# Kernel optimization log

Measured on AMD Instinct MI355X. Metric: run time of the kernel, lower is better.

Reference implementation:

```python
import jax, jax.numpy as jnp
import numpy as np

M, IN, OUT = 8192, 4096, 4096
BLOCK_N, BLOCK_K = 128, 128
NB = IN // BLOCK_K  # 32 in-blocks
INT8_MAX = 127.0
EPS = 1e-6


def setup_inputs() -> dict:
    key = jax.random.key(0)
    k1, k2, k3, k4 = jax.random.split(key, 4)
    x = jax.random.normal(k1, (M, IN), dtype=jnp.float32)
    # pre-quantized int8 weights, layout [output_size, input_size]
    weight_q = jax.random.randint(k2, (OUT, IN), -128, 128, dtype=jnp.int8)
    # block-wise scales, kernel-ready layout [in_blocks, 1, output_size]
    weight_scale = (jax.random.uniform(k3, (NB, 1, OUT), dtype=jnp.float32) + 0.5) * 0.01
    bias = jax.random.normal(k4, (OUT,), dtype=jnp.float32)
    return {"x": x, "weight_q": weight_q, "weight_scale": weight_scale, "bias": bias}


def _quantize_activation(x):
    # dynamic per-token symmetric int8 quantization
    amax = jnp.max(jnp.abs(x), axis=-1, keepdims=True)          # [M, 1]
    x_scale = jnp.maximum(amax, EPS) / INT8_MAX                  # [M, 1]
    x_q = jnp.clip(jnp.round(x / x_scale), -128.0, 127.0)        # [M, IN]
    return x_q, x_scale


def reference(x, weight_q, weight_scale, bias):
    # x: [M, IN]; weight_q: [OUT, IN] int8; weight_scale: [NB, 1, OUT]; bias: [OUT]
    x_q, x_scale = _quantize_activation(x)
    # Dequantize weights block-wise along K: scale for column k, row n is
    # weight_scale[k // BLOCK_K, 0, n].
    ws = weight_scale[:, 0, :].T                                 # [OUT, NB]
    w_deq = (weight_q.astype(jnp.float32).reshape(OUT, NB, BLOCK_K)
             * ws[:, :, None]).reshape(OUT, IN)                  # [OUT, IN] fp32
    # quantized matmul + dequant by activation scale
    out = jnp.einsum('mk,nk->mn', x_q, w_deq) * x_scale          # [M, OUT]
    out = out + bias
    return out
```

## Files before the change

### kernel.cpp

```cpp
#include <hip/hip_runtime.h>
#include <cstdint>

#define M_DIM 8192
#define K_DIM 4096
#define N_DIM 4096
#define NKT   32

typedef int   v4i  __attribute__((ext_vector_type(4)));
typedef int   v16i __attribute__((ext_vector_type(16)));
typedef float v4f  __attribute__((ext_vector_type(4)));

__device__ __forceinline__ void gload_lds16(const void* g, void* l) {
  __builtin_amdgcn_global_load_lds(
      (const __attribute__((address_space(1))) void*)g,
      (__attribute__((address_space(3))) void*)l, 16, 0, 0);
}

__global__ __launch_bounds__(256) void pack_w(
    const int* __restrict__ w32, int* __restrict__ w8) {
  const size_t i = (size_t)blockIdx.x * 256 + threadIdx.x;
  const int4 v = ((const int4*)w32)[i];
  w8[i] = (v.x & 255) | ((v.y & 255) << 8) | ((v.z & 255) << 16) | ((v.w & 255) << 24);
}

__global__ __launch_bounds__(256) void quant_rows(
    const float* __restrict__ x, int8_t* __restrict__ xq, float* __restrict__ xs) {
  const int row = blockIdx.x;
  const int tid = threadIdx.x;
  const float4* xr = (const float4*)(x + (size_t)row * K_DIM);

  float4 v[4];
  float amax = 0.f;
#pragma unroll
  for (int i = 0; i < 4; ++i) {
    v[i] = xr[i * 256 + tid];
    amax = fmaxf(amax, fmaxf(fmaxf(fabsf(v[i].x), fabsf(v[i].y)),
                             fmaxf(fabsf(v[i].z), fabsf(v[i].w))));
  }
#pragma unroll
  for (int off = 32; off > 0; off >>= 1)
    amax = fmaxf(amax, __shfl_xor(amax, off, 64));

  __shared__ float red[4];
  if ((tid & 63) == 0) red[tid >> 6] = amax;
  __syncthreads();
  amax = fmaxf(fmaxf(red[0], red[1]), fmaxf(red[2], red[3]));
  amax = fmaxf(amax, 1e-6f);
  const float s   = amax / 127.0f;
  const float inv = 127.0f / amax;
  if (tid == 0) xs[row] = s;

  int* xqo = (int*)(xq + (size_t)row * K_DIM);
#pragma unroll
  for (int i = 0; i < 4; ++i) {
    int q0 = (int)fminf(fmaxf(rintf(v[i].x * inv), -128.f), 127.f);
    int q1 = (int)fminf(fmaxf(rintf(v[i].y * inv), -128.f), 127.f);
    int q2 = (int)fminf(fmaxf(rintf(v[i].z * inv), -128.f), 127.f);
    int q3 = (int)fminf(fmaxf(rintf(v[i].w * inv), -128.f), 127.f);
    xqo[i * 256 + tid] =
        (q0 & 255) | ((q1 & 255) << 8) | ((q2 & 255) << 16) | ((q3 & 255) << 24);
  }
}

__global__ __launch_bounds__(512, 2) void gemm_q8(
    const int8_t* __restrict__ xq, const int8_t* __restrict__ wq,
    const float* __restrict__ wscale, const float* __restrict__ xs,
    const float* __restrict__ bias, float* __restrict__ out) {
  __shared__ int8_t lA[2][32768];
  __shared__ int8_t lB[2][32768];

  const int tid = threadIdx.x;
  const int m0 = blockIdx.x * 256;
  const int n0 = blockIdx.y * 256;

  const int srow   = tid >> 3;
  const int schunk = (tid & 7) ^ (srow & 7);
  const int8_t* ga = xq + (size_t)(m0 + srow) * K_DIM + schunk * 16;
  const int8_t* gb = wq + (size_t)(n0 + srow) * K_DIM + schunk * 16;

  const int lane = tid & 63;
  const int wv  = tid >> 6;
  const int wm  = (wv >> 2) << 7;
  const int wn  = (wv & 3) << 6;
  const int l31 = lane & 31;
  const int hi  = lane >> 5;

  int swz[4];
#pragma unroll
  for (int k = 0; k < 4; ++k) swz[k] = (((2 * k + hi) ^ (lane & 7)) << 4);
  const int aoff = (wm + l31) << 7;
  const int boff = (wn + l31) << 7;

  float facc[4][2][16];
#pragma unroll
  for (int i = 0; i < 4; ++i)
#pragma unroll
    for (int j = 0; j < 2; ++j)
#pragma unroll
      for (int r = 0; r < 16; ++r) facc[i][j][r] = 0.f;

  const float* wsp = wscale + n0 + wn + l31;

#pragma unroll
  for (int h = 0; h < 2; ++h)
#pragma unroll
    for (int p = 0; p < 2; ++p) {
      const size_t go = (size_t)(h * 128 + p * 64) * K_DIM;
      const int lo = h * 16384 + p * 8192 + tid * 16;
      gload_lds16(ga + go, &lA[0][lo]);
      gload_lds16(gb + go, &lB[0][lo]);
    }
  __syncthreads();

  for (int kt = 0; kt < NKT; ++kt) {
    const int d = kt & 1;
    const int kn = (kt + 1) & (NKT - 1);
    const int8_t* gan = ga + (size_t)kn * 128;
    const int8_t* gbn = gb + (size_t)kn * 128;
    int8_t* lan = &lA[d ^ 1][0];
    int8_t* lbn = &lB[d ^ 1][0];
    const int8_t* pa = &lA[d][0];
    const int8_t* pb = &lB[d][0];

    const float ws0 = wsp[(size_t)kt * N_DIM];
    const float ws1 = wsp[(size_t)kt * N_DIM + 32];

    v4i bfr[2][4];
#pragma unroll
    for (int j = 0; j < 2; ++j)
#pragma unroll
      for (int k = 0; k < 4; ++k)
        bfr[j][k] = *(const v4i*)(pb + boff + j * 4096 + swz[k]);

    v4i acur[4];
#pragma unroll
    for (int k = 0; k < 4; ++k)
      acur[k] = *(const v4i*)(pa + aoff + swz[k]);

#pragma unroll
    for (int h = 0; h < 2; ++h)
#pragma unroll
      for (int p = 0; p < 2; ++p) {
        const size_t go = (size_t)(h * 128 + p * 64) * K_DIM;
        const int lo = h * 16384 + p * 8192 + tid * 16;
        gload_lds16(gan + go, lan + lo);
        gload_lds16(gbn + go, lbn + lo);
      }

#pragma unroll
    for (int i = 0; i < 4; ++i) {
      v4i anxt[4];
      if (i < 3) {
#pragma unroll
        for (int k = 0; k < 4; ++k)
          anxt[k] = *(const v4i*)(pa + aoff + (i + 1) * 4096 + swz[k]);
      }

      v16i ic0 = {};
      v16i ic1 = {};
      __builtin_amdgcn_s_setprio(1);
#pragma unroll
      for (int k = 0; k < 4; ++k) {
        ic0 = __builtin_amdgcn_mfma_i32_32x32x32_i8(acur[k], bfr[0][k], ic0, 0, 0, 0);
        ic1 = __builtin_amdgcn_mfma_i32_32x32x32_i8(acur[k], bfr[1][k], ic1, 0, 0, 0);
      }
      __builtin_amdgcn_s_setprio(0);

#pragma unroll
      for (int r = 0; r < 16; ++r) facc[i][0][r] += ws0 * (float)ic0[r];
#pragma unroll
      for (int r = 0; r < 16; ++r) facc[i][1][r] += ws1 * (float)ic1[r];

      if (i < 3) {
#pragma unroll
        for (int k = 0; k < 4; ++k) acur[k] = anxt[k];
      }
    }

    __syncthreads();
  }

  const float bv0 = bias[n0 + wn + l31];
  const float bv1 = bias[n0 + wn + 32 + l31];
#pragma unroll
  for (int i = 0; i < 4; ++i) {
    const int rbase = m0 + wm + i * 32 + (hi << 2);
#pragma unroll
    for (int q = 0; q < 4; ++q) {
      const v4f xv = *(const v4f*)(xs + rbase + q * 8);
#pragma unroll
      for (int r4 = 0; r4 < 4; ++r4) {
        const int r = q * 4 + r4;
        float* op = out + (size_t)(rbase + q * 8 + r4) * N_DIM + n0 + wn + l31;
        op[0]  = facc[i][0][r] * xv[r4] + bv0;
        op[32] = facc[i][1][r] * xv[r4] + bv1;
      }
    }
  }
}

extern "C" void kernel_launch(void* const* d_in, const int* in_sizes, int n_in,
                              void* d_out, int out_size, void* d_ws, size_t ws_size,
                              hipStream_t stream) {
  const float* x      = (const float*)d_in[0];
  const int*   w32    = (const int*)d_in[1];
  const float* wscale = (const float*)d_in[2];
  const float* bias   = (const float*)d_in[3];
  float* out = (float*)d_out;

  int8_t* xq  = (int8_t*)d_ws;
  int8_t* wq8 = (int8_t*)d_ws + (size_t)M_DIM * K_DIM;
  float*  xs  = (float*)((char*)d_ws + (size_t)M_DIM * K_DIM + (size_t)N_DIM * K_DIM);

  pack_w<<<(N_DIM * (size_t)K_DIM / 4 + 255) / 256, 256, 0, stream>>>(w32, (int*)wq8);
  quant_rows<<<M_DIM, 256, 0, stream>>>(x, xq, xs);
  dim3 grid(M_DIM / 256, N_DIM / 256);
  gemm_q8<<<grid, 512, 0, stream>>>(xq, wq8, wscale, xs, bias, out);
}
```

Before: 440.0 us.

## Pre-swizzle operands into MFMA fragment layout and load B directly to registers

```diff
diff --git a/kernel.cpp b/kernel.cpp
--- a/kernel.cpp
+++ b/kernel.cpp
@@ -16,49 +16,65 @@
       (__attribute__((address_space(3))) void*)l, 16, 0, 0);
 }
 
-__global__ __launch_bounds__(256) void pack_w(
-    const int* __restrict__ w32, int* __restrict__ w8) {
-  const size_t i = (size_t)blockIdx.x * 256 + threadIdx.x;
-  const int4 v = ((const int4*)w32)[i];
-  w8[i] = (v.x & 255) | ((v.y & 255) << 8) | ((v.z & 255) << 16) | ((v.w & 255) << 24);
-}
-
-__global__ __launch_bounds__(256) void quant_rows(
-    const float* __restrict__ x, int8_t* __restrict__ xq, float* __restrict__ xs) {
-  const int row = blockIdx.x;
+
+__global__ __launch_bounds__(256) void prep(
+    const float* __restrict__ x, const int* __restrict__ w32,
+    int8_t* __restrict__ xq, float* __restrict__ xs, int8_t* __restrict__ wq) {
   const int tid = threadIdx.x;
-  const float4* xr = (const float4*)(x + (size_t)row * K_DIM);
-
-  float4 v[4];
-  float amax = 0.f;
-#pragma unroll
-  for (int i = 0; i < 4; ++i) {
-    v[i] = xr[i * 256 + tid];
-    amax = fmaxf(amax, fmaxf(fmaxf(fabsf(v[i].x), fabsf(v[i].y)),
-                             fmaxf(fabsf(v[i].z), fabsf(v[i].w))));
-  }
-#pragma unroll
-  for (int off = 32; off > 0; off >>= 1)
-    amax = fmaxf(amax, __shfl_xor(amax, off, 64));
-
-  __shared__ float red[4];
-  if ((tid & 63) == 0) red[tid >> 6] = amax;
-  __syncthreads();
-  amax = fmaxf(fmaxf(red[0], red[1]), fmaxf(red[2], red[3]));
-  amax = fmaxf(amax, 1e-6f);
-  const float s   = amax / 127.0f;
-  const float inv = 127.0f / amax;
-  if (tid == 0) xs[row] = s;
-
-  int* xqo = (int*)(xq + (size_t)row * K_DIM);
-#pragma unroll
-  for (int i = 0; i < 4; ++i) {
-    int q0 = (int)fminf(fmaxf(rintf(v[i].x * inv), -128.f), 127.f);
-    int q1 = (int)fminf(fmaxf(rintf(v[i].y * inv), -128.f), 127.f);
-    int q2 = (int)fminf(fmaxf(rintf(v[i].z * inv), -128.f), 127.f);
-    int q3 = (int)fminf(fmaxf(rintf(v[i].w * inv), -128.f), 127.f);
-    xqo[i * 256 + tid] =
-        (q0 & 255) | ((q1 & 255) << 8) | ((q2 & 255) << 16) | ((q3 & 255) << 24);
+  if (blockIdx.x < M_DIM) {
+    const int row = blockIdx.x;
+    const float4* xr = (const float4*)(x + (size_t)row * K_DIM);
+    float4 v[4];
+    float amax = 0.f;
+#pragma unroll
+    for (int i = 0; i < 4; ++i) {
+      v[i] = xr[tid * 4 + i];
+      amax = fmaxf(amax, fmaxf(fmaxf(fabsf(v[i].x), fabsf(v[i].y)),
+                               fmaxf(fabsf(v[i].z), fabsf(v[i].w))));
+    }
+#pragma unroll
+    for (int off = 32; off > 0; off >>= 1)
+      amax = fmaxf(amax, __shfl_xor(amax, off, 64));
+    __shared__ float red[4];
+    if ((tid & 63) == 0) red[tid >> 6] = amax;
+    __syncthreads();
+    amax = fmaxf(fmaxf(red[0], red[1]), fmaxf(red[2], red[3]));
+    amax = fmaxf(amax, 1e-6f);
+    const float s   = amax / 127.0f;
+    const float inv = 127.0f / amax;
+    if (tid == 0) xs[row] = s;
+
+    int w[4];
+#pragma unroll
+    for (int i = 0; i < 4; ++i) {
+      int q0 = (int)fminf(fmaxf(rintf(v[i].x * inv), -128.f), 127.f);
+      int q1 = (int)fminf(fmaxf(rintf(v[i].y * inv), -128.f), 127.f);
+      int q2 = (int)fminf(fmaxf(rintf(v[i].z * inv), -128.f), 127.f);
+      int q3 = (int)fminf(fmaxf(rintf(v[i].w * inv), -128.f), 127.f);
+      w[i] = (q0 & 255) | ((q1 & 255) << 8) | ((q2 & 255) << 16) | ((q3 & 255) << 24);
+    }
+    const int kt = tid >> 3, c = tid & 7;
+    const size_t doff =
+        ((((size_t)(row >> 5) * 32 + kt) * 4 + (c >> 1)) * 64 + (row & 31) + 32 * (c & 1)) * 16;
+    v4i ov = {w[0], w[1], w[2], w[3]};
+    *(v4i*)(xq + doff) = ov;
+  } else {
+    const size_t t = (size_t)(blockIdx.x - M_DIM) * 256 + tid;
+    const int l   = (int)(t & 63);
+    const int k   = (int)((t >> 6) & 3);
+    const int kt  = (int)((t >> 8) & 31);
+    const int n32 = (int)(t >> 13);
+    const int row = n32 * 32 + (l & 31);
+    const int col = kt * 128 + (2 * k + (l >> 5)) * 16;
+    const int4* src = (const int4*)(w32 + (size_t)row * K_DIM + col);
+    int o[4];
+#pragma unroll
+    for (int q = 0; q < 4; ++q) {
+      const int4 e = src[q];
+      o[q] = (e.x & 255) | ((e.y & 255) << 8) | ((e.z & 255) << 16) | ((e.w & 255) << 24);
+    }
+    v4i ov = {o[0], o[1], o[2], o[3]};
+    *(v4i*)(wq + t * 16) = ov;
   }
 }
 
@@ -67,29 +83,26 @@
     const float* __restrict__ wscale, const float* __restrict__ xs,
     const float* __restrict__ bias, float* __restrict__ out) {
   __shared__ int8_t lA[2][32768];
-  __shared__ int8_t lB[2][32768];
 
   const int tid = threadIdx.x;
+  const int lane = tid & 63;
+  const int wv = tid >> 6;
   const int m0 = blockIdx.x * 256;
   const int n0 = blockIdx.y * 256;
-
-  const int srow   = tid >> 3;
-  const int schunk = (tid & 7) ^ (srow & 7);
-  const int8_t* ga = xq + (size_t)(m0 + srow) * K_DIM + schunk * 16;
-  const int8_t* gb = wq + (size_t)(n0 + srow) * K_DIM + schunk * 16;
-
-  const int lane = tid & 63;
-  const int wv  = tid >> 6;
-  const int wm  = (wv >> 2) << 7;
-  const int wn  = (wv & 3) << 6;
+  const int wm = (wv >> 2) << 7;
+  const int wn = (wv & 3) << 6;
   const int l31 = lane & 31;
-  const int hi  = lane >> 5;
-
-  int swz[4];
-#pragma unroll
-  for (int k = 0; k < 4; ++k) swz[k] = (((2 * k + hi) ^ (lane & 7)) << 4);
-  const int aoff = (wm + l31) << 7;
-  const int boff = (wn + l31) << 7;
+  const int hi = lane >> 5;
+
+  const size_t stageBase =
+      ((size_t)((m0 >> 5) + (tid >> 6))) * 131072 + (size_t)(tid & 63) * 16;
+  const int dstoff = (tid >> 6) * 4096 + (tid & 63) * 16;
+
+  const int n32_0 = (n0 >> 5) + ((wv & 3) << 1);
+  const int8_t* gb0 = wq + (size_t)n32_0 * 131072 + lane * 16;
+  const int8_t* gb1 = gb0 + 131072;
+
+  const int aBase = ((wv >> 2) * 4) * 4096 + lane * 16;
 
   float facc[4][2][16];
 #pragma unroll
@@ -102,50 +115,34 @@
   const float* wsp = wscale + n0 + wn + l31;
 
 #pragma unroll
-  for (int h = 0; h < 2; ++h)
-#pragma unroll
-    for (int p = 0; p < 2; ++p) {
-      const size_t go = (size_t)(h * 128 + p * 64) * K_DIM;
-      const int lo = h * 16384 + p * 8192 + tid * 16;
-      gload_lds16(ga + go, &lA[0][lo]);
-      gload_lds16(gb + go, &lB[0][lo]);
-    }
+  for (int p = 0; p < 4; ++p)
+    gload_lds16(xq + stageBase + (size_t)p * 1024, &lA[0][dstoff + p * 1024]);
+  v4i bcur[2][4];
+#pragma unroll
+  for (int k = 0; k < 4; ++k) {
+    bcur[0][k] = *(const v4i*)(gb0 + k * 1024);
+    bcur[1][k] = *(const v4i*)(gb1 + k * 1024);
+  }
+  float ws0 = wsp[0];
+  float ws1 = wsp[32];
   __syncthreads();
 
   for (int kt = 0; kt < NKT; ++kt) {
     const int d = kt & 1;
     const int kn = (kt + 1) & (NKT - 1);
-    const int8_t* gan = ga + (size_t)kn * 128;
-    const int8_t* gbn = gb + (size_t)kn * 128;
-    int8_t* lan = &lA[d ^ 1][0];
-    int8_t* lbn = &lB[d ^ 1][0];
-    const int8_t* pa = &lA[d][0];
-    const int8_t* pb = &lB[d][0];
-
-    const float ws0 = wsp[(size_t)kt * N_DIM];
-    const float ws1 = wsp[(size_t)kt * N_DIM + 32];
-
-    v4i bfr[2][4];
-#pragma unroll
-    for (int j = 0; j < 2; ++j)
-#pragma unroll
-      for (int k = 0; k < 4; ++k)
-        bfr[j][k] = *(const v4i*)(pb + boff + j * 4096 + swz[k]);
+
+#pragma unroll
+    for (int p = 0; p < 4; ++p)
+      gload_lds16(xq + stageBase + (size_t)kn * 4096 + (size_t)p * 1024,
+                  &lA[d ^ 1][dstoff + p * 1024]);
+    __builtin_amdgcn_sched_barrier(0);
+
+    const float cw0 = ws0, cw1 = ws1;
+    const int8_t* pa = &lA[d][aBase];
 
     v4i acur[4];
 #pragma unroll
-    for (int k = 0; k < 4; ++k)
-      acur[k] = *(const v4i*)(pa + aoff + swz[k]);
-
-#pragma unroll
-    for (int h = 0; h < 2; ++h)
-#pragma unroll
-      for (int p = 0; p < 2; ++p) {
-        const size_t go = (size_t)(h * 128 + p * 64) * K_DIM;
-        const int lo = h * 16384 + p * 8192 + tid * 16;
-        gload_lds16(gan + go, lan + lo);
-        gload_lds16(gbn + go, lbn + lo);
-      }
+    for (int k = 0; k < 4; ++k) acur[k] = *(const v4i*)(pa + k * 1024);
 
 #pragma unroll
     for (int i = 0; i < 4; ++i) {
@@ -153,31 +150,39 @@
       if (i < 3) {
 #pragma unroll
         for (int k = 0; k < 4; ++k)
-          anxt[k] = *(const v4i*)(pa + aoff + (i + 1) * 4096 + swz[k]);
-      }
-
+          anxt[k] = *(const v4i*)(pa + (i + 1) * 4096 + k * 1024);
+      }
       v16i ic0 = {};
       v16i ic1 = {};
       __builtin_amdgcn_s_setprio(1);
 #pragma unroll
       for (int k = 0; k < 4; ++k) {
-        ic0 = __builtin_amdgcn_mfma_i32_32x32x32_i8(acur[k], bfr[0][k], ic0, 0, 0, 0);
-        ic1 = __builtin_amdgcn_mfma_i32_32x32x32_i8(acur[k], bfr[1][k], ic1, 0, 0, 0);
+        ic0 = __builtin_amdgcn_mfma_i32_32x32x32_i8(acur[k], bcur[0][k], ic0, 0, 0, 0);
+        ic1 = __builtin_amdgcn_mfma_i32_32x32x32_i8(acur[k], bcur[1][k], ic1, 0, 0, 0);
       }
       __builtin_amdgcn_s_setprio(0);
-
-#pragma unroll
-      for (int r = 0; r < 16; ++r) facc[i][0][r] += ws0 * (float)ic0[r];
-#pragma unroll
-      for (int r = 0; r < 16; ++r) facc[i][1][r] += ws1 * (float)ic1[r];
-
+#pragma unroll
+      for (int r = 0; r < 16; ++r) facc[i][0][r] += cw0 * (float)ic0[r];
+#pragma unroll
+      for (int r = 0; r < 16; ++r) facc[i][1][r] += cw1 * (float)ic1[r];
       if (i < 3) {
 #pragma unroll
         for (int k = 0; k < 4; ++k) acur[k] = anxt[k];
       }
     }
 
-    __syncthreads();
+#pragma unroll
+    for (int k = 0; k < 4; ++k) {
+      bcur[0][k] = *(const v4i*)(gb0 + (size_t)kn * 4096 + k * 1024);
+      bcur[1][k] = *(const v4i*)(gb1 + (size_t)kn * 4096 + k * 1024);
+    }
+    ws0 = wsp[(size_t)kn * N_DIM];
+    ws1 = wsp[(size_t)kn * N_DIM + 32];
+
+    __builtin_amdgcn_sched_barrier(0);
+    asm volatile("s_waitcnt vmcnt(10)" ::: "memory");
+    __builtin_amdgcn_s_barrier();
+    __builtin_amdgcn_sched_barrier(0);
   }
 
   const float bv0 = bias[n0 + wn + l31];
@@ -212,8 +217,8 @@
   int8_t* wq8 = (int8_t*)d_ws + (size_t)M_DIM * K_DIM;
   float*  xs  = (float*)((char*)d_ws + (size_t)M_DIM * K_DIM + (size_t)N_DIM * K_DIM);
 
-  pack_w<<<(N_DIM * (size_t)K_DIM / 4 + 255) / 256, 256, 0, stream>>>(w32, (int*)wq8);
-  quant_rows<<<M_DIM, 256, 0, stream>>>(x, xq, xs);
+  const int packBlocks = (int)((size_t)N_DIM * K_DIM / 16 / 256);
+  prep<<<M_DIM + packBlocks, 256, 0, stream>>>(x, w32, xq, xs, wq8);
   dim3 grid(M_DIM / 256, N_DIM / 256);
   gemm_q8<<<grid, 512, 0, stream>>>(xq, wq8, wscale, xs, bias, out);
 }
```

New measurement: 446.0 us. Within noise of the previous version (+1.4%).
